# Optimization experiments

Measured on AMD Instinct MI355X. Metric: run time of the kernel, lower is better.

Reference implementation:

```python
import jax, jax.numpy as jnp
import numpy as np

N = 50000
E = 250000
NUM_ETYPES = 4
H = 2  # num_heads
EPS = 1e-12


def _gat_conv(x, W, al, ar, b, src, dst):
    # x: (N, in_dim); W: (in_dim, H*D); al/ar/b: (H, D); src/dst: (E,)
    D = al.shape[-1]
    feat = (x @ W).reshape(-1, H, D)            # (N, H, D)
    el = jnp.sum(feat * al, axis=-1)            # (N, H)
    er = jnp.sum(feat * ar, axis=-1)            # (N, H)
    e = jax.nn.leaky_relu(el[src] + er[dst], 0.2)   # (E, H)
    emax = jax.ops.segment_max(e, dst, num_segments=N)
    ex = jnp.exp(e - emax[dst])
    denom = jax.ops.segment_sum(ex, dst, num_segments=N)
    alpha = ex / denom[dst]                     # (E, H) segment softmax over in-edges
    msg = feat[src] * alpha[:, :, None]         # (E, H, D)
    out = jax.ops.segment_sum(msg, dst, num_segments=N)  # (N, H, D)
    return out + b


def _hetero_layer(x, W, al, ar, b, edges):
    # vmap GATConv over the edge-type axis, then HeteroGraphConv aggregate='mean'
    outs = jax.vmap(lambda w, a, r, bb, e: _gat_conv(x, w, a, r, bb, e[0], e[1]))(
        W, al, ar, b, edges)                    # (T, N, H, D)
    return jnp.mean(outs, axis=0)               # (N, H, D)


def _post(v):
    # relu -> F.normalize(dim=1, i.e. across heads) -> dropout(eval: identity) -> mean over heads
    v = jax.nn.relu(v)
    norm = jnp.sqrt(jnp.sum(v * v, axis=1, keepdims=True))
    v = v / jnp.maximum(norm, EPS)
    return jnp.mean(v, axis=1)                  # (N, D)


def setup_inputs() -> dict:
    key = jax.random.key(0)
    ks = jax.random.split(key, 16)
    s = 0.05
    inp = {
        'x': jax.random.normal(ks[0], (N, 23), jnp.float32),
        'edges': jax.random.randint(ks[1], (NUM_ETYPES, 2, E), 0, N, jnp.int32),
        'W0': jax.random.normal(ks[2], (NUM_ETYPES, 23, H * 64), jnp.float32) * s,
        'al0': jax.random.normal(ks[3], (NUM_ETYPES, H, 64), jnp.float32) * s,
        'ar0': jax.random.normal(ks[4], (NUM_ETYPES, H, 64), jnp.float32) * s,
        'b0': jnp.zeros((NUM_ETYPES, H, 64), jnp.float32),
        'W1': jax.random.normal(ks[5], (NUM_ETYPES, 64, H * 64), jnp.float32) * s,
        'al1': jax.random.normal(ks[6], (NUM_ETYPES, H, 64), jnp.float32) * s,
        'ar1': jax.random.normal(ks[7], (NUM_ETYPES, H, 64), jnp.float32) * s,
        'b1': jnp.zeros((NUM_ETYPES, H, 64), jnp.float32),
        'W2': jax.random.normal(ks[8], (NUM_ETYPES, 64, H * 64), jnp.float32) * s,
        'al2': jax.random.normal(ks[9], (NUM_ETYPES, H, 64), jnp.float32) * s,
        'ar2': jax.random.normal(ks[10], (NUM_ETYPES, H, 64), jnp.float32) * s,
        'b2': jnp.zeros((NUM_ETYPES, H, 64), jnp.float32),
    }
    return inp


def reference(x, edges, W0, al0, ar0, b0, W1, al1, ar1, b1, W2, al2, ar2, b2):
    h = x  # feature_by_level, feat_level=0
    h = _post(_hetero_layer(h, W0, al0, ar0, b0, edges))
    h = _post(_hetero_layer(h, W1, al1, ar1, b1, edges))
    h = jnp.mean(_hetero_layer(h, W2, al2, ar2, b2, edges), axis=1)  # (N, out_dim)
    out = jnp.mean(h, axis=0, keepdims=True)    # dgl.mean_nodes, single graph -> (1, out_dim)
    return out
```

## Files before the change

### kernel.cpp

```cpp
#include <hip/hip_runtime.h>

#define NN 50000
#define NE 250000
#define NSCAN_BLKS ((NN + 255)/256)
#define EDGE_BLKS ((4*NE + 255)/256)

typedef __attribute__((ext_vector_type(8))) short bf16x8;
typedef __attribute__((ext_vector_type(4))) float f32x4;

__device__ inline ushort f2bf(float f) {
  uint u = __float_as_uint(f);
  return (ushort)((u + 0x7fffu + ((u >> 16) & 1u)) >> 16);
}
__device__ inline float bf2f(ushort b) { return __uint_as_float(((uint)b) << 16); }

__global__ __launch_bounds__(256) void zero_ints(int* __restrict__ p, int n) {
  int i = blockIdx.x*256 + threadIdx.x;
  if (i < n) p[i] = 0;
}
__global__ __launch_bounds__(256) void zero_floats(float* __restrict__ p, int n) {
  int i = blockIdx.x*256 + threadIdx.x;
  if (i < n) p[i] = 0.f;
}

__global__ __launch_bounds__(256) void count_kernel(const int* __restrict__ edges, int* __restrict__ counts) {
  int idx = blockIdx.x*256 + threadIdx.x;
  if (idx >= 4*NE) return;
  int t = idx / NE, e = idx - t*NE;
  int dst = edges[(size_t)t*2*NE + NE + e];
  atomicAdd(&counts[t*NN + dst], 1);
}

__global__ __launch_bounds__(256) void sumdeg_kernel(const int* __restrict__ counts, int* __restrict__ totdeg) {
  int v = blockIdx.x*256 + threadIdx.x;
  if (v < NN) totdeg[v] = counts[v] + counts[NN+v] + counts[2*NN+v] + counts[3*NN+v];
}

__global__ __launch_bounds__(256) void scan1_kernel(const int* __restrict__ in, int* __restrict__ out, int* __restrict__ bsum, int n) {
  __shared__ int sd[256];
  int i = blockIdx.x*256 + threadIdx.x;
  int v = (i < n) ? in[i] : 0;
  sd[threadIdx.x] = v;
  __syncthreads();
  for (int off = 1; off < 256; off <<= 1) {
    int add = (threadIdx.x >= off) ? sd[threadIdx.x - off] : 0;
    __syncthreads();
    sd[threadIdx.x] += add;
    __syncthreads();
  }
  if (i < n) out[i] = sd[threadIdx.x] - v;
  if (threadIdx.x == 255) bsum[blockIdx.x] = sd[255];
}

__global__ __launch_bounds__(1024) void scan2_kernel(int* __restrict__ bsum, int nb) {
  __shared__ int sd[1024];
  int i = threadIdx.x;
  int v = (i < nb) ? bsum[i] : 0;
  sd[i] = v;
  __syncthreads();
  for (int off = 1; off < 1024; off <<= 1) {
    int add = (i >= off) ? sd[i - off] : 0;
    __syncthreads();
    sd[i] += add;
    __syncthreads();
  }
  if (i < nb) bsum[i] = sd[i] - v;
}

__global__ __launch_bounds__(256) void scan3b_kernel(int* __restrict__ rp, const int* __restrict__ bsum, int n, int total) {
  int i = blockIdx.x*256 + threadIdx.x;
  if (i < n) rp[i] += bsum[blockIdx.x];
  if (i == 0) rp[n] = total;
}

__global__ __launch_bounds__(256) void make_cursor_kernel(const int* __restrict__ rp2, const int* __restrict__ counts,
                                                          int* __restrict__ cursor, int* __restrict__ sub_ptr) {
  int v = blockIdx.x*256 + threadIdx.x;
  if (v >= NN) return;
  int b = rp2[v];
  int s1 = b  + counts[v];
  int s2 = s1 + counts[NN+v];
  int s3 = s2 + counts[2*NN+v];
  cursor[v] = b; cursor[NN+v] = s1; cursor[2*NN+v] = s2; cursor[3*NN+v] = s3;
  sub_ptr[NN+v] = s1; sub_ptr[2*NN+v] = s2; sub_ptr[3*NN+v] = s3;
}

__global__ __launch_bounds__(256) void scatter2_kernel(const int* __restrict__ edges, int* __restrict__ cursor,
                                                       int* __restrict__ col2) {
  int idx = blockIdx.x*256 + threadIdx.x;
  if (idx >= 4*NE) return;
  int t = idx / NE, e = idx - t*NE;
  int src = edges[(size_t)t*2*NE + e];
  int dst = edges[(size_t)t*2*NE + NE + e];
  int pos = atomicAdd(&cursor[t*NN + dst], 1);
  col2[pos] = t*NN + src;
}

__global__ __launch_bounds__(256) void convert_x_kernel(const float* __restrict__ x, ushort* __restrict__ xpad) {
  int i = blockIdx.x*256 + threadIdx.x;
  if (i >= NN*64) return;
  int k = i & 63, n = i >> 6;
  xpad[i] = (k < 23) ? f2bf(x[n*23 + k]) : (ushort)0;
}

__global__ __launch_bounds__(256) void convert_wt2_kernel(const float* __restrict__ W, const float* __restrict__ al,
                                                          const float* __restrict__ ar, ushort* __restrict__ WTg2, int Kin) {
  int i = blockIdx.x*256 + threadIdx.x;
  if (i >= 4*144*64) return;
  int k = i & 63; int c = (i >> 6) % 144; int t = i / (144*64);
  float val = 0.f;
  if (c < 128) {
    val = (k < Kin) ? W[((size_t)t*Kin + k)*128 + c] : 0.f;
  } else if (c < 132 && k < Kin) {
    int m = c - 128, h = m & 1;
    const float* A = ((m < 2) ? al : ar) + t*128 + h*64;
    const float* wrow = W + ((size_t)t*Kin + k)*128 + h*64;
    float s = 0.f;
    for (int c2 = 0; c2 < 64; ++c2) s += wrow[c2]*A[c2];
    val = s;
  }
  WTg2[((size_t)t*144 + c)*64 + k] = f2bf(val);
}

__global__ __launch_bounds__(256)
void gemm_mfma_kernel(const ushort* __restrict__ hbf,
                      const ushort* __restrict__ WTg2,
                      uint* __restrict__ featu,
                      float* __restrict__ elp, float* __restrict__ erp)
{
  __shared__ ushort WT[144*64];
  const int t = blockIdx.y;
  const int tid = threadIdx.x;
  const int wv = tid >> 6, lane = tid & 63;
  const int node0 = blockIdx.x*64;

  {
    const ushort* src = WTg2 + (size_t)t*144*64;
    for (int i = tid; i < 1152; i += 256) {
      int c = i >> 3, jj = i & 7;
      bf16x8 val = *(const bf16x8*)(src + (size_t)c*64 + jj*8);
      *(bf16x8*)((char*)WT + c*128 + ((jj ^ (c & 7))*16)) = val;
    }
  }
  __syncthreads();

  const int mrow = lane & 15;
  const int kq = lane >> 4;
  const int anode = node0 + wv*16 + mrow;

  const bf16x8 a0 = *(const bf16x8*)(hbf + (size_t)anode*64 + kq*8);
  const bf16x8 a1 = *(const bf16x8*)(hbf + (size_t)anode*64 + 32 + kq*8);

  f32x4 acc[9];
  #pragma unroll
  for (int nb = 0; nb < 9; ++nb) acc[nb] = (f32x4){0.f,0.f,0.f,0.f};

  #pragma unroll
  for (int nb = 0; nb < 9; ++nb) {
    const int c = nb*16 + mrow;
    const bf16x8 b0 = *(const bf16x8*)((const char*)WT + c*128 + ((kq       ^ (c&7))*16));
    const bf16x8 b1 = *(const bf16x8*)((const char*)WT + c*128 + (((4 + kq) ^ (c&7))*16));
    acc[nb] = __builtin_amdgcn_mfma_f32_16x16x32_bf16(a0, b0, acc[nb], 0, 0, 0);
    acc[nb] = __builtin_amdgcn_mfma_f32_16x16x32_bf16(a1, b1, acc[nb], 0, 0, 0);
  }

  const int noder = node0 + wv*16 + kq*4;
  #pragma unroll
  for (int nb = 0; nb < 4; ++nb) {
    const int d = nb*16 + mrow;
    #pragma unroll
    for (int r = 0; r < 4; ++r) {
      if (noder + r < NN) {
        const uint pk = (uint)f2bf(acc[nb][r]) | ((uint)f2bf(acc[nb+4][r]) << 16);
        featu[((size_t)t*NN + noder + r)*64 + d] = pk;
      }
    }
  }
  if (mrow < 4) {
    const int h = mrow & 1;
    float* dstp = (mrow < 2) ? elp : erp;
    #pragma unroll
    for (int r = 0; r < 4; ++r) {
      if (noder + r < NN)
        dstp[((size_t)t*NN + noder + r)*2 + h] = acc[8][r];
    }
  }
}

__global__ __launch_bounds__(256)
void gather_kernel(const uint* __restrict__ featu, const float* __restrict__ elp,
                   const float* __restrict__ erp, const int* __restrict__ col2,
                   const int* __restrict__ row_ptr2, const int* __restrict__ sub_ptr,
                   const float* __restrict__ ball, ushort* __restrict__ hout, int post)
{
  const int v = __builtin_amdgcn_readfirstlane(blockIdx.x*4 + (threadIdx.x >> 6));
  const int lane = threadIdx.x & 63;

  const int b0 = row_ptr2[v];
  const int b4 = row_ptr2[v+1];
  const int s1 = sub_ptr[NN+v], s2 = sub_ptr[2*NN+v], s3 = sub_ptr[3*NN+v];
  const int bounds[5] = {b0, s1, s2, s3, b4};

  float ax = 0.f, ay = 0.f;

  #pragma unroll
  for (int t = 0; t < 4; ++t) {
    const int lo = bounds[t], hi = bounds[t+1];
    if (lo >= hi) continue;
    const float2 er2 = ((const float2*)erp)[(size_t)t*NN + v];
    float sum0 = 0.f, sum1 = 0.f, tx = 0.f, ty = 0.f;
    #pragma unroll 4
    for (int q = lo; q < hi; ++q) {
      const int c = col2[q];
      const float2 e2 = ((const float2*)elp)[c];
      float u0 = e2.x + er2.x, u1 = e2.y + er2.y;
      u0 = (u0 > 0.f) ? u0 : 0.2f*u0;
      u1 = (u1 > 0.f) ? u1 : 0.2f*u1;
      const float p0 = __expf(fminf(fmaxf(u0, -60.f), 60.f));
      const float p1 = __expf(fminf(fmaxf(u1, -60.f), 60.f));
      sum0 += p0; sum1 += p1;
      const uint w = featu[(uint)c*64u + (uint)lane];
      tx += p0 * __uint_as_float(w << 16);
      ty += p1 * __uint_as_float(w & 0xffff0000u);
    }
    ax += tx * __builtin_amdgcn_rcpf(sum0);
    ay += ty * __builtin_amdgcn_rcpf(sum1);
  }

  float bx = 0.f, by = 0.f;
  #pragma unroll
  for (int t = 0; t < 4; ++t) { bx += ball[t*128 + lane]; by += ball[t*128 + 64 + lane]; }
  ax = 0.25f*(ax + bx); ay = 0.25f*(ay + by);

  float o;
  if (post) {
    ax = fmaxf(ax, 0.f); ay = fmaxf(ay, 0.f);
    o = 0.5f*(ax + ay) / fmaxf(sqrtf(ax*ax + ay*ay), 1e-12f);
  } else {
    o = 0.5f*(ax + ay);
  }
  hout[(size_t)v*64 + lane] = f2bf(o);
}

__global__ __launch_bounds__(256) void reduce_nodes(const ushort* __restrict__ hn, float* __restrict__ accum) {
  __shared__ float sd[256];
  int d = threadIdx.x & 63, rg = threadIdx.x >> 6;
  float s = 0.f;
  for (int r = blockIdx.x*4 + rg; r < NN; r += gridDim.x*4) s += bf2f(hn[(size_t)r*64 + d]);
  sd[threadIdx.x] = s;
  __syncthreads();
  if (threadIdx.x < 64) {
    s = sd[threadIdx.x] + sd[threadIdx.x+64] + sd[threadIdx.x+128] + sd[threadIdx.x+192];
    atomicAdd(&accum[threadIdx.x], s);
  }
}
__global__ __launch_bounds__(64) void final_out_kernel(const float* __restrict__ accum, float* __restrict__ out) {
  int d = threadIdx.x;
  if (d < 64) out[d] = accum[d] * (1.0f/NN);
}

extern "C" void kernel_launch(void* const* d_in, const int* in_sizes, int n_in,
                              void* d_out, int out_size, void* d_ws, size_t ws_size,
                              hipStream_t stream) {
  const float* x     = (const float*)d_in[0];
  const int*   edges = (const int*)d_in[1];
  const float* W[3]  = {(const float*)d_in[2], (const float*)d_in[6], (const float*)d_in[10]};
  const float* al[3] = {(const float*)d_in[3], (const float*)d_in[7], (const float*)d_in[11]};
  const float* ar[3] = {(const float*)d_in[4], (const float*)d_in[8], (const float*)d_in[12]};
  const float* b[3]  = {(const float*)d_in[5], (const float*)d_in[9], (const float*)d_in[13]};

  char* ws = (char*)d_ws;
  auto up = [](size_t x_) { return (x_ + 255) & ~(size_t)255; };

  const size_t szFeat = (size_t)4*NN*64*sizeof(uint);
  const size_t szElp  = (size_t)4*NN*2*sizeof(float);
  const size_t szCol  = (size_t)4*NE*sizeof(int);
  const size_t szHB   = (size_t)(NN+64)*64*sizeof(ushort);
  const size_t szWT   = (size_t)4*144*64*sizeof(ushort);
  const size_t szI4   = (size_t)4*NN*sizeof(int);
  const size_t szI1   = (size_t)(NN+1)*sizeof(int);

  size_t o = 0;
  uint*   featu  = (uint*)(ws + o);   o += up(szFeat);
  float*  elp    = (float*)(ws + o);  o += up(szElp);
  float*  erp    = (float*)(ws + o);  o += up(szElp);
  int*    col2   = (int*)(ws + o);    o += up(szCol);
  ushort* xpad   = (ushort*)(ws + o); o += up(szHB);
  ushort* hbuf   = (ushort*)(ws + o); o += up(szHB);
  ushort* WTg2   = (ushort*)(ws + o); o += up(szWT);
  float*  accum  = (float*)(ws + o);  o += up(256);
  int* row_ptr2  = (int*)(ws + o);    o += up(szI1);
  int* totdeg    = (int*)(ws + o);    o += up(szI1);
  int* cursor    = (int*)(ws + o);    o += up(szI4);
  int* counts    = (int*)(ws + o);    o += up(szI4);
  int* sub_ptr   = (int*)(ws + o);    o += up(szI4);
  int* bsum      = (int*)(ws + o);    o += up(4096);

  zero_ints<<<(4*NN + 255)/256, 256, 0, stream>>>(counts, 4*NN);
  count_kernel<<<EDGE_BLKS, 256, 0, stream>>>(edges, counts);
  sumdeg_kernel<<<NSCAN_BLKS, 256, 0, stream>>>(counts, totdeg);
  scan1_kernel<<<NSCAN_BLKS, 256, 0, stream>>>(totdeg, row_ptr2, bsum, NN);
  scan2_kernel<<<1, 1024, 0, stream>>>(bsum, NSCAN_BLKS);
  scan3b_kernel<<<NSCAN_BLKS, 256, 0, stream>>>(row_ptr2, bsum, NN, 4*NE);
  make_cursor_kernel<<<NSCAN_BLKS, 256, 0, stream>>>(row_ptr2, counts, cursor, sub_ptr);
  scatter2_kernel<<<EDGE_BLKS, 256, 0, stream>>>(edges, cursor, col2);

  convert_x_kernel<<<(NN*64 + 255)/256, 256, 0, stream>>>(x, xpad);

  const int gemmGX = (NN + 63)/64;

  for (int l = 0; l < 3; ++l) {
    const ushort* hin = (l == 0) ? xpad : hbuf;
    convert_wt2_kernel<<<(4*144*64 + 255)/256, 256, 0, stream>>>(W[l], al[l], ar[l], WTg2, (l == 0) ? 23 : 64);
    gemm_mfma_kernel<<<dim3(gemmGX, 4), 256, 0, stream>>>(hin, WTg2, featu, elp, erp);
    gather_kernel<<<NN/4, 256, 0, stream>>>(featu, elp, erp, col2, row_ptr2, sub_ptr, b[l], hbuf, (l < 2) ? 1 : 0);
  }

  zero_floats<<<1, 64, 0, stream>>>(accum, 64);
  reduce_nodes<<<256, 256, 0, stream>>>(hbuf, accum);
  final_out_kernel<<<1, 64, 0, stream>>>(accum, (float*)d_out);
}
```

Baseline: 409.5 us.

## Replace CSR build with per-destination linked lists via atomicExch

The count/scan/scatter CSR construction pipeline (eight kernels) is replaced by a fill plus a single link kernel that builds per-(edge type, destination) linked lists with atomicExch. The gather kernel now walks four lists per node at once, interleaving the edge types to overlap their dependent loads. This cuts preprocessing launches and passes over the edge array, but each gather step becomes a pointer chase (nxt then edges then features) with serialized latency, repeated in all three layers.

```diff
diff --git a/kernel.cpp b/kernel.cpp
--- a/kernel.cpp
+++ b/kernel.cpp
@@ -2,7 +2,6 @@
 
 #define NN 50000
 #define NE 250000
-#define NSCAN_BLKS ((NN + 255)/256)
 #define EDGE_BLKS ((4*NE + 255)/256)
 
 typedef __attribute__((ext_vector_type(8))) short bf16x8;
@@ -14,86 +13,22 @@
 }
 __device__ inline float bf2f(ushort b) { return __uint_as_float(((uint)b) << 16); }
 
-__global__ __launch_bounds__(256) void zero_ints(int* __restrict__ p, int n) {
-  int i = blockIdx.x*256 + threadIdx.x;
-  if (i < n) p[i] = 0;
+__global__ __launch_bounds__(256) void fill_ints(int* __restrict__ p, int n, int val) {
+  int i = blockIdx.x*256 + threadIdx.x;
+  if (i < n) p[i] = val;
 }
 __global__ __launch_bounds__(256) void zero_floats(float* __restrict__ p, int n) {
   int i = blockIdx.x*256 + threadIdx.x;
   if (i < n) p[i] = 0.f;
 }
 
-__global__ __launch_bounds__(256) void count_kernel(const int* __restrict__ edges, int* __restrict__ counts) {
+__global__ __launch_bounds__(256) void link_kernel(const int* __restrict__ edges,
+                                                   int* __restrict__ head, int* __restrict__ nxt) {
   int idx = blockIdx.x*256 + threadIdx.x;
   if (idx >= 4*NE) return;
   int t = idx / NE, e = idx - t*NE;
   int dst = edges[(size_t)t*2*NE + NE + e];
-  atomicAdd(&counts[t*NN + dst], 1);
-}
-
-__global__ __launch_bounds__(256) void sumdeg_kernel(const int* __restrict__ counts, int* __restrict__ totdeg) {
-  int v = blockIdx.x*256 + threadIdx.x;
-  if (v < NN) totdeg[v] = counts[v] + counts[NN+v] + counts[2*NN+v] + counts[3*NN+v];
-}
-
-__global__ __launch_bounds__(256) void scan1_kernel(const int* __restrict__ in, int* __restrict__ out, int* __restrict__ bsum, int n) {
-  __shared__ int sd[256];
-  int i = blockIdx.x*256 + threadIdx.x;
-  int v = (i < n) ? in[i] : 0;
-  sd[threadIdx.x] = v;
-  __syncthreads();
-  for (int off = 1; off < 256; off <<= 1) {
-    int add = (threadIdx.x >= off) ? sd[threadIdx.x - off] : 0;
-    __syncthreads();
-    sd[threadIdx.x] += add;
-    __syncthreads();
-  }
-  if (i < n) out[i] = sd[threadIdx.x] - v;
-  if (threadIdx.x == 255) bsum[blockIdx.x] = sd[255];
-}
-
-__global__ __launch_bounds__(1024) void scan2_kernel(int* __restrict__ bsum, int nb) {
-  __shared__ int sd[1024];
-  int i = threadIdx.x;
-  int v = (i < nb) ? bsum[i] : 0;
-  sd[i] = v;
-  __syncthreads();
-  for (int off = 1; off < 1024; off <<= 1) {
-    int add = (i >= off) ? sd[i - off] : 0;
-    __syncthreads();
-    sd[i] += add;
-    __syncthreads();
-  }
-  if (i < nb) bsum[i] = sd[i] - v;
-}
-
-__global__ __launch_bounds__(256) void scan3b_kernel(int* __restrict__ rp, const int* __restrict__ bsum, int n, int total) {
-  int i = blockIdx.x*256 + threadIdx.x;
-  if (i < n) rp[i] += bsum[blockIdx.x];
-  if (i == 0) rp[n] = total;
-}
-
-__global__ __launch_bounds__(256) void make_cursor_kernel(const int* __restrict__ rp2, const int* __restrict__ counts,
-                                                          int* __restrict__ cursor, int* __restrict__ sub_ptr) {
-  int v = blockIdx.x*256 + threadIdx.x;
-  if (v >= NN) return;
-  int b = rp2[v];
-  int s1 = b  + counts[v];
-  int s2 = s1 + counts[NN+v];
-  int s3 = s2 + counts[2*NN+v];
-  cursor[v] = b; cursor[NN+v] = s1; cursor[2*NN+v] = s2; cursor[3*NN+v] = s3;
-  sub_ptr[NN+v] = s1; sub_ptr[2*NN+v] = s2; sub_ptr[3*NN+v] = s3;
-}
-
-__global__ __launch_bounds__(256) void scatter2_kernel(const int* __restrict__ edges, int* __restrict__ cursor,
-                                                       int* __restrict__ col2) {
-  int idx = blockIdx.x*256 + threadIdx.x;
-  if (idx >= 4*NE) return;
-  int t = idx / NE, e = idx - t*NE;
-  int src = edges[(size_t)t*2*NE + e];
-  int dst = edges[(size_t)t*2*NE + NE + e];
-  int pos = atomicAdd(&cursor[t*NN + dst], 1);
-  col2[pos] = t*NN + src;
+  nxt[idx] = atomicExch(&head[t*NN + dst], e);
 }
 
 __global__ __launch_bounds__(256) void convert_x_kernel(const float* __restrict__ x, ushort* __restrict__ xpad) {
@@ -189,42 +124,54 @@
 
 __global__ __launch_bounds__(256)
 void gather_kernel(const uint* __restrict__ featu, const float* __restrict__ elp,
-                   const float* __restrict__ erp, const int* __restrict__ col2,
-                   const int* __restrict__ row_ptr2, const int* __restrict__ sub_ptr,
+                   const float* __restrict__ erp, const int* __restrict__ edges,
+                   const int* __restrict__ head, const int* __restrict__ nxt,
                    const float* __restrict__ ball, ushort* __restrict__ hout, int post)
 {
   const int v = __builtin_amdgcn_readfirstlane(blockIdx.x*4 + (threadIdx.x >> 6));
   const int lane = threadIdx.x & 63;
-
-  const int b0 = row_ptr2[v];
-  const int b4 = row_ptr2[v+1];
-  const int s1 = sub_ptr[NN+v], s2 = sub_ptr[2*NN+v], s3 = sub_ptr[3*NN+v];
-  const int bounds[5] = {b0, s1, s2, s3, b4};
+  const float2* elp2 = (const float2*)elp;
+  const float2* erp2 = (const float2*)erp;
+
+  int e[4];
+  float sum0[4], sum1[4], tx[4], ty[4];
+  float2 er2[4];
+  #pragma unroll
+  for (int t = 0; t < 4; ++t) {
+    e[t] = __builtin_amdgcn_readfirstlane(head[t*NN + v]);
+    er2[t] = erp2[(size_t)t*NN + v];
+    sum0[t] = 0.f; sum1[t] = 0.f; tx[t] = 0.f; ty[t] = 0.f;
+  }
+
+  while (e[0] >= 0 || e[1] >= 0 || e[2] >= 0 || e[3] >= 0) {
+    #pragma unroll
+    for (int t = 0; t < 4; ++t) {
+      if (e[t] >= 0) {
+        const int idx = e[t];
+        const int src = __builtin_amdgcn_readfirstlane(edges[(size_t)t*2*NE + idx]);
+        const int nx  = __builtin_amdgcn_readfirstlane(nxt[(size_t)t*NE + idx]);
+        const float2 e2 = elp2[(size_t)t*NN + src];
+        const uint w = featu[((uint)t*NN + (uint)src)*64u + (uint)lane];
+        float u0 = e2.x + er2[t].x, u1 = e2.y + er2[t].y;
+        u0 = (u0 > 0.f) ? u0 : 0.2f*u0;
+        u1 = (u1 > 0.f) ? u1 : 0.2f*u1;
+        const float p0 = __expf(fminf(fmaxf(u0, -60.f), 60.f));
+        const float p1 = __expf(fminf(fmaxf(u1, -60.f), 60.f));
+        sum0[t] += p0; sum1[t] += p1;
+        tx[t] += p0 * __uint_as_float(w << 16);
+        ty[t] += p1 * __uint_as_float(w & 0xffff0000u);
+        e[t] = nx;
+      }
+    }
+  }
 
   float ax = 0.f, ay = 0.f;
-
   #pragma unroll
   for (int t = 0; t < 4; ++t) {
-    const int lo = bounds[t], hi = bounds[t+1];
-    if (lo >= hi) continue;
-    const float2 er2 = ((const float2*)erp)[(size_t)t*NN + v];
-    float sum0 = 0.f, sum1 = 0.f, tx = 0.f, ty = 0.f;
-    #pragma unroll 4
-    for (int q = lo; q < hi; ++q) {
-      const int c = col2[q];
-      const float2 e2 = ((const float2*)elp)[c];
-      float u0 = e2.x + er2.x, u1 = e2.y + er2.y;
-      u0 = (u0 > 0.f) ? u0 : 0.2f*u0;
-      u1 = (u1 > 0.f) ? u1 : 0.2f*u1;
-      const float p0 = __expf(fminf(fmaxf(u0, -60.f), 60.f));
-      const float p1 = __expf(fminf(fmaxf(u1, -60.f), 60.f));
-      sum0 += p0; sum1 += p1;
-      const uint w = featu[(uint)c*64u + (uint)lane];
-      tx += p0 * __uint_as_float(w << 16);
-      ty += p1 * __uint_as_float(w & 0xffff0000u);
-    }
-    ax += tx * __builtin_amdgcn_rcpf(sum0);
-    ay += ty * __builtin_amdgcn_rcpf(sum1);
+    if (sum0[t] > 0.f) {
+      ax += tx[t] * __builtin_amdgcn_rcpf(sum0[t]);
+      ay += ty[t] * __builtin_amdgcn_rcpf(sum1[t]);
+    }
   }
 
   float bx = 0.f, by = 0.f;
@@ -274,36 +221,24 @@
 
   const size_t szFeat = (size_t)4*NN*64*sizeof(uint);
   const size_t szElp  = (size_t)4*NN*2*sizeof(float);
-  const size_t szCol  = (size_t)4*NE*sizeof(int);
   const size_t szHB   = (size_t)(NN+64)*64*sizeof(ushort);
   const size_t szWT   = (size_t)4*144*64*sizeof(ushort);
-  const size_t szI4   = (size_t)4*NN*sizeof(int);
-  const size_t szI1   = (size_t)(NN+1)*sizeof(int);
+  const size_t szHead = (size_t)4*NN*sizeof(int);
+  const size_t szNxt  = (size_t)4*NE*sizeof(int);
 
   size_t o = 0;
   uint*   featu  = (uint*)(ws + o);   o += up(szFeat);
   float*  elp    = (float*)(ws + o);  o += up(szElp);
   float*  erp    = (float*)(ws + o);  o += up(szElp);
-  int*    col2   = (int*)(ws + o);    o += up(szCol);
   ushort* xpad   = (ushort*)(ws + o); o += up(szHB);
   ushort* hbuf   = (ushort*)(ws + o); o += up(szHB);
   ushort* WTg2   = (ushort*)(ws + o); o += up(szWT);
   float*  accum  = (float*)(ws + o);  o += up(256);
-  int* row_ptr2  = (int*)(ws + o);    o += up(szI1);
-  int* totdeg    = (int*)(ws + o);    o += up(szI1);
-  int* cursor    = (int*)(ws + o);    o += up(szI4);
-  int* counts    = (int*)(ws + o);    o += up(szI4);
-  int* sub_ptr   = (int*)(ws + o);    o += up(szI4);
-  int* bsum      = (int*)(ws + o);    o += up(4096);
-
-  zero_ints<<<(4*NN + 255)/256, 256, 0, stream>>>(counts, 4*NN);
-  count_kernel<<<EDGE_BLKS, 256, 0, stream>>>(edges, counts);
-  sumdeg_kernel<<<NSCAN_BLKS, 256, 0, stream>>>(counts, totdeg);
-  scan1_kernel<<<NSCAN_BLKS, 256, 0, stream>>>(totdeg, row_ptr2, bsum, NN);
-  scan2_kernel<<<1, 1024, 0, stream>>>(bsum, NSCAN_BLKS);
-  scan3b_kernel<<<NSCAN_BLKS, 256, 0, stream>>>(row_ptr2, bsum, NN, 4*NE);
-  make_cursor_kernel<<<NSCAN_BLKS, 256, 0, stream>>>(row_ptr2, counts, cursor, sub_ptr);
-  scatter2_kernel<<<EDGE_BLKS, 256, 0, stream>>>(edges, cursor, col2);
+  int*    head   = (int*)(ws + o);    o += up(szHead);
+  int*    nxt    = (int*)(ws + o);    o += up(szNxt);
+
+  fill_ints<<<(4*NN + 255)/256, 256, 0, stream>>>(head, 4*NN, -1);
+  link_kernel<<<EDGE_BLKS, 256, 0, stream>>>(edges, head, nxt);
 
   convert_x_kernel<<<(NN*64 + 255)/256, 256, 0, stream>>>(x, xpad);
 
@@ -313,7 +248,7 @@
     const ushort* hin = (l == 0) ? xpad : hbuf;
     convert_wt2_kernel<<<(4*144*64 + 255)/256, 256, 0, stream>>>(W[l], al[l], ar[l], WTg2, (l == 0) ? 23 : 64);
     gemm_mfma_kernel<<<dim3(gemmGX, 4), 256, 0, stream>>>(hin, WTg2, featu, elp, erp);
-    gather_kernel<<<NN/4, 256, 0, stream>>>(featu, elp, erp, col2, row_ptr2, sub_ptr, b[l], hbuf, (l < 2) ? 1 : 0);
+    gather_kernel<<<NN/4, 256, 0, stream>>>(featu, elp, erp, edges, head, nxt, b[l], hbuf, (l < 2) ? 1 : 0);
   }
 
   zero_floats<<<1, 64, 0, stream>>>(accum, 64);
```

After: 492.9 us. 20.4% more time.

## Aggregate raw inputs before projection and bucket edge scatter by destination

Applied to the files above, without the earlier changes.

The GAT layer is reordered to aggregate the input features per edge type first (attention logits come from precomputed W·al and W·ar vectors), then apply W in a single MFMA transform kernel. That kernel sums the four edge types, adds bias and applies the post-processing. The gather now reads a 64-wide bf16 input row per edge instead of a packed 2-head feature row. In exchange it writes a large per-type aggregate buffer (4·N·128 bf16) that the transform reads back. The edge scatter is also split into destination-range buckets to localize atomics, at the cost of reading the edge list four times.

```diff
diff --git a/kernel.cpp b/kernel.cpp
--- a/kernel.cpp
+++ b/kernel.cpp
@@ -4,6 +4,8 @@
 #define NE 250000
 #define NSCAN_BLKS ((NN + 255)/256)
 #define EDGE_BLKS ((4*NE + 255)/256)
+#define NBUCK 4
+#define BSZ ((NN + NBUCK - 1)/NBUCK)
 
 typedef __attribute__((ext_vector_type(8))) short bf16x8;
 typedef __attribute__((ext_vector_type(4))) float f32x4;
@@ -85,15 +87,17 @@
   sub_ptr[NN+v] = s1; sub_ptr[2*NN+v] = s2; sub_ptr[3*NN+v] = s3;
 }
 
-__global__ __launch_bounds__(256) void scatter2_kernel(const int* __restrict__ edges, int* __restrict__ cursor,
-                                                       int* __restrict__ col2) {
-  int idx = blockIdx.x*256 + threadIdx.x;
+__global__ __launch_bounds__(256) void scatter_bucketed(const int* __restrict__ edges, int* __restrict__ cursor,
+                                                        int* __restrict__ col2) {
+  const int b = blockIdx.x / EDGE_BLKS;
+  const int idx = (blockIdx.x - b*EDGE_BLKS)*256 + threadIdx.x;
   if (idx >= 4*NE) return;
-  int t = idx / NE, e = idx - t*NE;
-  int src = edges[(size_t)t*2*NE + e];
-  int dst = edges[(size_t)t*2*NE + NE + e];
-  int pos = atomicAdd(&cursor[t*NN + dst], 1);
-  col2[pos] = t*NN + src;
+  const int t = idx / NE, e = idx - t*NE;
+  const int dst = edges[(size_t)t*2*NE + NE + e];
+  if (dst < b*BSZ || dst >= (b+1)*BSZ) return;
+  const int src = edges[(size_t)t*2*NE + e];
+  const int pos = atomicAdd(&cursor[t*NN + dst], 1);
+  col2[pos] = src;
 }
 
 __global__ __launch_bounds__(256) void convert_x_kernel(const float* __restrict__ x, ushort* __restrict__ xpad) {
@@ -103,143 +107,170 @@
   xpad[i] = (k < 23) ? f2bf(x[n*23 + k]) : (ushort)0;
 }
 
-__global__ __launch_bounds__(256) void convert_wt2_kernel(const float* __restrict__ W, const float* __restrict__ al,
-                                                          const float* __restrict__ ar, ushort* __restrict__ WTg2, int Kin) {
-  int i = blockIdx.x*256 + threadIdx.x;
-  if (i >= 4*144*64) return;
-  int k = i & 63; int c = (i >> 6) % 144; int t = i / (144*64);
-  float val = 0.f;
-  if (c < 128) {
-    val = (k < Kin) ? W[((size_t)t*Kin + k)*128 + c] : 0.f;
-  } else if (c < 132 && k < Kin) {
-    int m = c - 128, h = m & 1;
-    const float* A = ((m < 2) ? al : ar) + t*128 + h*64;
-    const float* wrow = W + ((size_t)t*Kin + k)*128 + h*64;
-    float s = 0.f;
-    for (int c2 = 0; c2 < 64; ++c2) s += wrow[c2]*A[c2];
-    val = s;
-  }
-  WTg2[((size_t)t*144 + c)*64 + k] = f2bf(val);
+__global__ __launch_bounds__(256) void convert_wb_kernel(const float* __restrict__ W, ushort* __restrict__ WB, int Kin) {
+  int i = blockIdx.x*256 + threadIdx.x;
+  if (i >= 4*128*64) return;
+  int k = i & 63, c = (i >> 6) & 127, t = i >> 13;
+  float w = (k < Kin) ? W[((size_t)t*Kin + k)*128 + c] : 0.f;
+  WB[i] = f2bf(w);
+}
+
+__global__ __launch_bounds__(256) void walwar_kernel(const float* __restrict__ W, const float* __restrict__ al,
+                                                     const float* __restrict__ ar, ushort* __restrict__ wwb, int Kin) {
+  int i = blockIdx.x*256 + threadIdx.x;
+  if (i >= 16*64) return;
+  int c = i >> 6, k = i & 63;
+  int lr = c >> 3, t = (c >> 1) & 3, h = c & 1;
+  float v = 0.f;
+  if (k < Kin) {
+    const float* A = (lr ? ar : al) + t*128 + h*64;
+    const float* wr = W + ((size_t)t*Kin + k)*128 + h*64;
+    for (int d = 0; d < 64; ++d) v += wr[d]*A[d];
+  }
+  wwb[i] = f2bf(v);
 }
 
 __global__ __launch_bounds__(256)
-void gemm_mfma_kernel(const ushort* __restrict__ hbf,
-                      const ushort* __restrict__ WTg2,
-                      uint* __restrict__ featu,
-                      float* __restrict__ elp, float* __restrict__ erp)
+void elk_kernel(const ushort* __restrict__ hbf, const ushort* __restrict__ wwb,
+                float* __restrict__ elp, float* __restrict__ erp)
 {
-  __shared__ ushort WT[144*64];
-  const int t = blockIdx.y;
+  __shared__ ushort BS[16*64];
+  __shared__ float sC[16*66];
   const int tid = threadIdx.x;
+  if (tid < 128) ((bf16x8*)BS)[tid] = ((const bf16x8*)wwb)[tid];
+  __syncthreads();
+
   const int wv = tid >> 6, lane = tid & 63;
-  const int node0 = blockIdx.x*64;
-
-  {
-    const ushort* src = WTg2 + (size_t)t*144*64;
-    for (int i = tid; i < 1152; i += 256) {
-      int c = i >> 3, jj = i & 7;
-      bf16x8 val = *(const bf16x8*)(src + (size_t)c*64 + jj*8);
-      *(bf16x8*)((char*)WT + c*128 + ((jj ^ (c & 7))*16)) = val;
-    }
-  }
-  __syncthreads();
-
-  const int mrow = lane & 15;
-  const int kq = lane >> 4;
-  const int anode = node0 + wv*16 + mrow;
+  const int mrow = lane & 15, kq = lane >> 4;
+  const int anode = blockIdx.x*64 + wv*16 + mrow;
 
   const bf16x8 a0 = *(const bf16x8*)(hbf + (size_t)anode*64 + kq*8);
   const bf16x8 a1 = *(const bf16x8*)(hbf + (size_t)anode*64 + 32 + kq*8);
-
-  f32x4 acc[9];
+  const bf16x8 b0 = *(const bf16x8*)(BS + mrow*64 + kq*8);
+  const bf16x8 b1 = *(const bf16x8*)(BS + mrow*64 + 32 + kq*8);
+
+  f32x4 acc = (f32x4){0.f,0.f,0.f,0.f};
+  acc = __builtin_amdgcn_mfma_f32_16x16x32_bf16(a0, b0, acc, 0, 0, 0);
+  acc = __builtin_amdgcn_mfma_f32_16x16x32_bf16(a1, b1, acc, 0, 0, 0);
+
   #pragma unroll
-  for (int nb = 0; nb < 9; ++nb) acc[nb] = (f32x4){0.f,0.f,0.f,0.f};
+  for (int r = 0; r < 4; ++r) sC[mrow*66 + wv*16 + kq*4 + r] = acc[r];
+  __syncthreads();
+
+  const int t = tid >> 6, n = tid & 63;
+  const int node = blockIdx.x*64 + n;
+  if (node < NN) {
+    float2 e2 = make_float2(sC[(t*2+0)*66 + n], sC[(t*2+1)*66 + n]);
+    float2 r2 = make_float2(sC[(8+t*2+0)*66 + n], sC[(8+t*2+1)*66 + n]);
+    ((float2*)elp)[(size_t)t*NN + node] = e2;
+    ((float2*)erp)[(size_t)t*NN + node] = r2;
+  }
+}
+
+__global__ __launch_bounds__(256)
+void gather_kernel(const ushort* __restrict__ hbf, const float* __restrict__ elp,
+                   const float* __restrict__ erp, const int* __restrict__ col2,
+                   const int* __restrict__ row_ptr2, const int* __restrict__ sub_ptr,
+                   ushort* __restrict__ agg)
+{
+  const int v = __builtin_amdgcn_readfirstlane(blockIdx.x*4 + (threadIdx.x >> 6));
+  const int lane = threadIdx.x & 63;
+
+  const int b0 = row_ptr2[v];
+  const int b4 = row_ptr2[v+1];
+  const int s1 = sub_ptr[NN+v], s2 = sub_ptr[2*NN+v], s3 = sub_ptr[3*NN+v];
+  const int bounds[5] = {b0, s1, s2, s3, b4};
 
   #pragma unroll
-  for (int nb = 0; nb < 9; ++nb) {
-    const int c = nb*16 + mrow;
-    const bf16x8 b0 = *(const bf16x8*)((const char*)WT + c*128 + ((kq       ^ (c&7))*16));
-    const bf16x8 b1 = *(const bf16x8*)((const char*)WT + c*128 + (((4 + kq) ^ (c&7))*16));
-    acc[nb] = __builtin_amdgcn_mfma_f32_16x16x32_bf16(a0, b0, acc[nb], 0, 0, 0);
-    acc[nb] = __builtin_amdgcn_mfma_f32_16x16x32_bf16(a1, b1, acc[nb], 0, 0, 0);
+  for (int t = 0; t < 4; ++t) {
+    const int lo = bounds[t], hi = bounds[t+1];
+    float a0 = 0.f, a1 = 0.f;
+    if (lo < hi) {
+      const float2 er2 = ((const float2*)erp)[(size_t)t*NN + v];
+      float sum0 = 0.f, sum1 = 0.f;
+      for (int q = lo; q < hi; ++q) {
+        const int src = __builtin_amdgcn_readfirstlane(col2[q]);
+        const float2 e2 = ((const float2*)elp)[(size_t)t*NN + src];
+        float u0 = e2.x + er2.x, u1 = e2.y + er2.y;
+        u0 = (u0 > 0.f) ? u0 : 0.2f*u0;
+        u1 = (u1 > 0.f) ? u1 : 0.2f*u1;
+        const float p0 = __expf(fminf(fmaxf(u0, -60.f), 60.f));
+        const float p1 = __expf(fminf(fmaxf(u1, -60.f), 60.f));
+        sum0 += p0; sum1 += p1;
+        const float xv = bf2f(hbf[(size_t)src*64 + lane]);
+        a0 += p0*xv; a1 += p1*xv;
+      }
+      a0 *= __builtin_amdgcn_rcpf(sum0);
+      a1 *= __builtin_amdgcn_rcpf(sum1);
+    }
+    const size_t base = ((size_t)t*NN + v)*128;
+    agg[base + lane]      = f2bf(a0);
+    agg[base + 64 + lane] = f2bf(a1);
+  }
+}
+
+__global__ __launch_bounds__(256)
+void transform_kernel(const ushort* __restrict__ agg, const ushort* __restrict__ WB,
+                      const float* __restrict__ ball, ushort* __restrict__ hout, int post)
+{
+  __shared__ ushort WT[4*128*64];
+  __shared__ float sb[128];
+  const int tid = threadIdx.x;
+
+  for (int i = tid; i < 4096; i += 256) {
+    int row = i >> 3, jj = i & 7;
+    bf16x8 val = ((const bf16x8*)WB)[i];
+    *(bf16x8*)((char*)WT + row*128 + ((jj ^ (row & 7))*16)) = val;
+  }
+  if (tid < 128) sb[tid] = 0.25f*(ball[tid] + ball[128+tid] + ball[256+tid] + ball[384+tid]);
+  __syncthreads();
+
+  const int wv = tid >> 6, lane = tid & 63;
+  const int mrow = lane & 15, kq = lane >> 4;
+  const int node0 = blockIdx.x*64;
+  const int anode = node0 + wv*16 + mrow;
+
+  f32x4 acc[8];
+  #pragma unroll
+  for (int nb = 0; nb < 8; ++nb) acc[nb] = (f32x4){0.f,0.f,0.f,0.f};
+
+  for (int t = 0; t < 4; ++t) {
+    const ushort* ar_ = agg + ((size_t)t*NN + anode)*128;
+    const bf16x8 a00 = *(const bf16x8*)(ar_ + kq*8);
+    const bf16x8 a01 = *(const bf16x8*)(ar_ + 32 + kq*8);
+    const bf16x8 a10 = *(const bf16x8*)(ar_ + 64 + kq*8);
+    const bf16x8 a11 = *(const bf16x8*)(ar_ + 96 + kq*8);
+    #pragma unroll
+    for (int nb = 0; nb < 8; ++nb) {
+      const int row = t*128 + nb*16 + mrow;
+      const bf16x8 b0 = *(const bf16x8*)((const char*)WT + row*128 + ((kq       ^ (row&7))*16));
+      const bf16x8 b1 = *(const bf16x8*)((const char*)WT + row*128 + (((4 + kq) ^ (row&7))*16));
+      acc[nb] = __builtin_amdgcn_mfma_f32_16x16x32_bf16(nb < 4 ? a00 : a10, b0, acc[nb], 0, 0, 0);
+      acc[nb] = __builtin_amdgcn_mfma_f32_16x16x32_bf16(nb < 4 ? a01 : a11, b1, acc[nb], 0, 0, 0);
+    }
   }
 
   const int noder = node0 + wv*16 + kq*4;
   #pragma unroll
   for (int nb = 0; nb < 4; ++nb) {
     const int d = nb*16 + mrow;
+    const float bm0 = sb[d], bm1 = sb[64 + d];
     #pragma unroll
     for (int r = 0; r < 4; ++r) {
       if (noder + r < NN) {
-        const uint pk = (uint)f2bf(acc[nb][r]) | ((uint)f2bf(acc[nb+4][r]) << 16);
-        featu[((size_t)t*NN + noder + r)*64 + d] = pk;
+        float h0 = 0.25f*acc[nb][r]   + bm0;
+        float h1 = 0.25f*acc[nb+4][r] + bm1;
+        float o;
+        if (post) {
+          h0 = fmaxf(h0, 0.f); h1 = fmaxf(h1, 0.f);
+          o = 0.5f*(h0 + h1) / fmaxf(sqrtf(h0*h0 + h1*h1), 1e-12f);
+        } else {
+          o = 0.5f*(h0 + h1);
+        }
+        hout[(size_t)(noder + r)*64 + d] = f2bf(o);
       }
     }
   }
-  if (mrow < 4) {
-    const int h = mrow & 1;
-    float* dstp = (mrow < 2) ? elp : erp;
-    #pragma unroll
-    for (int r = 0; r < 4; ++r) {
-      if (noder + r < NN)
-        dstp[((size_t)t*NN + noder + r)*2 + h] = acc[8][r];
-    }
-  }
-}
-
-__global__ __launch_bounds__(256)
-void gather_kernel(const uint* __restrict__ featu, const float* __restrict__ elp,
-                   const float* __restrict__ erp, const int* __restrict__ col2,
-                   const int* __restrict__ row_ptr2, const int* __restrict__ sub_ptr,
-                   const float* __restrict__ ball, ushort* __restrict__ hout, int post)
-{
-  const int v = __builtin_amdgcn_readfirstlane(blockIdx.x*4 + (threadIdx.x >> 6));
-  const int lane = threadIdx.x & 63;
-
-  const int b0 = row_ptr2[v];
-  const int b4 = row_ptr2[v+1];
-  const int s1 = sub_ptr[NN+v], s2 = sub_ptr[2*NN+v], s3 = sub_ptr[3*NN+v];
-  const int bounds[5] = {b0, s1, s2, s3, b4};
-
-  float ax = 0.f, ay = 0.f;
-
-  #pragma unroll
-  for (int t = 0; t < 4; ++t) {
-    const int lo = bounds[t], hi = bounds[t+1];
-    if (lo >= hi) continue;
-    const float2 er2 = ((const float2*)erp)[(size_t)t*NN + v];
-    float sum0 = 0.f, sum1 = 0.f, tx = 0.f, ty = 0.f;
-    #pragma unroll 4
-    for (int q = lo; q < hi; ++q) {
-      const int c = col2[q];
-      const float2 e2 = ((const float2*)elp)[c];
-      float u0 = e2.x + er2.x, u1 = e2.y + er2.y;
-      u0 = (u0 > 0.f) ? u0 : 0.2f*u0;
-      u1 = (u1 > 0.f) ? u1 : 0.2f*u1;
-      const float p0 = __expf(fminf(fmaxf(u0, -60.f), 60.f));
-      const float p1 = __expf(fminf(fmaxf(u1, -60.f), 60.f));
-      sum0 += p0; sum1 += p1;
-      const uint w = featu[(uint)c*64u + (uint)lane];
-      tx += p0 * __uint_as_float(w << 16);
-      ty += p1 * __uint_as_float(w & 0xffff0000u);
-    }
-    ax += tx * __builtin_amdgcn_rcpf(sum0);
-    ay += ty * __builtin_amdgcn_rcpf(sum1);
-  }
-
-  float bx = 0.f, by = 0.f;
-  #pragma unroll
-  for (int t = 0; t < 4; ++t) { bx += ball[t*128 + lane]; by += ball[t*128 + 64 + lane]; }
-  ax = 0.25f*(ax + bx); ay = 0.25f*(ay + by);
-
-  float o;
-  if (post) {
-    ax = fmaxf(ax, 0.f); ay = fmaxf(ay, 0.f);
-    o = 0.5f*(ax + ay) / fmaxf(sqrtf(ax*ax + ay*ay), 1e-12f);
-  } else {
-    o = 0.5f*(ax + ay);
-  }
-  hout[(size_t)v*64 + lane] = f2bf(o);
 }
 
 __global__ __launch_bounds__(256) void reduce_nodes(const ushort* __restrict__ hn, float* __restrict__ accum) {
@@ -272,23 +303,25 @@
   char* ws = (char*)d_ws;
   auto up = [](size_t x_) { return (x_ + 255) & ~(size_t)255; };
 
-  const size_t szFeat = (size_t)4*NN*64*sizeof(uint);
+  const size_t szAgg  = ((size_t)4*NN + 64)*128*sizeof(ushort);
   const size_t szElp  = (size_t)4*NN*2*sizeof(float);
+  const size_t szHB   = (size_t)(NN+64)*64*sizeof(ushort);
+  const size_t szWB   = (size_t)4*128*64*sizeof(ushort);
+  const size_t szWWB  = (size_t)16*64*sizeof(ushort);
   const size_t szCol  = (size_t)4*NE*sizeof(int);
-  const size_t szHB   = (size_t)(NN+64)*64*sizeof(ushort);
-  const size_t szWT   = (size_t)4*144*64*sizeof(ushort);
   const size_t szI4   = (size_t)4*NN*sizeof(int);
   const size_t szI1   = (size_t)(NN+1)*sizeof(int);
 
   size_t o = 0;
-  uint*   featu  = (uint*)(ws + o);   o += up(szFeat);
+  ushort* agg    = (ushort*)(ws + o); o += up(szAgg);
   float*  elp    = (float*)(ws + o);  o += up(szElp);
   float*  erp    = (float*)(ws + o);  o += up(szElp);
-  int*    col2   = (int*)(ws + o);    o += up(szCol);
   ushort* xpad   = (ushort*)(ws + o); o += up(szHB);
   ushort* hbuf   = (ushort*)(ws + o); o += up(szHB);
-  ushort* WTg2   = (ushort*)(ws + o); o += up(szWT);
+  ushort* WB     = (ushort*)(ws + o); o += up(szWB);
+  ushort* wwb    = (ushort*)(ws + o); o += up(szWWB);
   float*  accum  = (float*)(ws + o);  o += up(256);
+  int*    col2   = (int*)(ws + o);    o += up(szCol);
   int* row_ptr2  = (int*)(ws + o);    o += up(szI1);
   int* totdeg    = (int*)(ws + o);    o += up(szI1);
   int* cursor    = (int*)(ws + o);    o += up(szI4);
@@ -303,7 +336,7 @@
   scan2_kernel<<<1, 1024, 0, stream>>>(bsum, NSCAN_BLKS);
   scan3b_kernel<<<NSCAN_BLKS, 256, 0, stream>>>(row_ptr2, bsum, NN, 4*NE);
   make_cursor_kernel<<<NSCAN_BLKS, 256, 0, stream>>>(row_ptr2, counts, cursor, sub_ptr);
-  scatter2_kernel<<<EDGE_BLKS, 256, 0, stream>>>(edges, cursor, col2);
+  scatter_bucketed<<<NBUCK*EDGE_BLKS, 256, 0, stream>>>(edges, cursor, col2);
 
   convert_x_kernel<<<(NN*64 + 255)/256, 256, 0, stream>>>(x, xpad);
 
@@ -311,9 +344,12 @@
 
   for (int l = 0; l < 3; ++l) {
     const ushort* hin = (l == 0) ? xpad : hbuf;
-    convert_wt2_kernel<<<(4*144*64 + 255)/256, 256, 0, stream>>>(W[l], al[l], ar[l], WTg2, (l == 0) ? 23 : 64);
-    gemm_mfma_kernel<<<dim3(gemmGX, 4), 256, 0, stream>>>(hin, WTg2, featu, elp, erp);
-    gather_kernel<<<NN/4, 256, 0, stream>>>(featu, elp, erp, col2, row_ptr2, sub_ptr, b[l], hbuf, (l < 2) ? 1 : 0);
+    const int Kin = (l == 0) ? 23 : 64;
+    convert_wb_kernel<<<(4*128*64 + 255)/256, 256, 0, stream>>>(W[l], WB, Kin);
+    walwar_kernel<<<(16*64 + 255)/256, 256, 0, stream>>>(W[l], al[l], ar[l], wwb, Kin);
+    elk_kernel<<<gemmGX, 256, 0, stream>>>(hin, wwb, elp, erp);
+    gather_kernel<<<NN/4, 256, 0, stream>>>(hin, elp, erp, col2, row_ptr2, sub_ptr, agg);
+    transform_kernel<<<gemmGX, 256, 0, stream>>>(agg, WB, b[l], hbuf, (l < 2) ? 1 : 0);
   }
 
   zero_floats<<<1, 64, 0, stream>>>(accum, 64);
```

New measurement: 457.7 us. 1.12x slower.
